# Performance work log

Measured on AMD Instinct MI355X. Metric: run time of the kernel, lower is better.

Reference implementation:

```python
import jax, jax.numpy as jnp
import numpy as np


def _rotate_half(x):
    a, b = jnp.split(x, 2, axis=-1)
    return jnp.concatenate([-b, a], axis=-1)


def _rope_tables(L, d, dtype):
    inv = 1.0 / (10000.0 ** (jnp.arange(0, d, 2, dtype=jnp.float32) / d))
    ang = jnp.arange(L, dtype=jnp.float32)[:, None] * inv[None, :]  # (L, d/2)
    cos = jnp.repeat(jnp.cos(ang), 2, axis=-1)[None, :, None, :].astype(dtype)  # (1,L,1,d)
    sin = jnp.repeat(jnp.sin(ang), 2, axis=-1)[None, :, None, :].astype(dtype)
    return cos, sin


def setup_inputs() -> dict:
    key = jax.random.key(0)
    ks = jax.random.split(key, 7)
    B, L, D, h = 1, 1024, 768, 12
    d = D // h
    s = 0.02
    return {
        "X": jax.random.normal(ks[0], (B, L, D), jnp.float32),
        "Wq": jax.random.normal(ks[1], (D, D), jnp.float32) * s,
        "Wk": jax.random.normal(ks[2], (D, D), jnp.float32) * s,
        "Wv": jax.random.normal(ks[3], (D, D), jnp.float32) * s,
        "Wu": jax.random.normal(ks[4], (D, D), jnp.float32) * s,
        "Wg": jax.random.normal(ks[5], (3 * h, D), jnp.float32) * s,
        "Wo": jax.random.normal(ks[6], (D, D), jnp.float32) * s,
        "prior_mu": jnp.zeros((1, 1, h, d), jnp.float32),
        "prior_log_tau": jnp.zeros((1, 1, h, 1), jnp.float32),
    }


def _forward(X, Wq, Wk, Wv, Wu, Wg, Wo, prior_mu, prior_log_tau):
    B, L, D = X.shape
    h = prior_mu.shape[2]
    d = D // h
    eps = 1e-12
    # projections (torch Linear: x @ W.T, no bias)
    q = (X @ Wq.T).reshape(B, L, h, d)
    k = (X @ Wk.T).reshape(B, L, h, d)
    v = (X @ Wv.T).reshape(B, L, h, d)
    u = (X @ Wu.T).reshape(B, L, h, d)
    gate = (X @ Wg.T).reshape(B, L, h, 3)
    t = jnp.arange(1, L + 1, dtype=X.dtype).reshape(1, L, 1, 1)
    # calculate_logit (logit_type='deviation', causal)
    log_tau = jnp.exp(jnp.clip(prior_log_tau, -50.0, 30.0))
    u_sum = jnp.cumsum(u, axis=1)
    bar_u = (log_tau * prior_mu + u_sum) / (log_tau + t)
    s_i = -jnp.sum(u * bar_u, axis=-1, keepdims=True) / np.float32(np.sqrt(d))  # (B,L,h,1)
    # RoPE + L2 normalize q, k
    cos, sin = _rope_tables(L, d, X.dtype)
    q = q * cos + _rotate_half(q) * sin
    k = k * cos + _rotate_half(k) * sin
    q = q / jnp.maximum(jnp.linalg.norm(q, axis=-1, keepdims=True), eps)
    k = k / jnp.maximum(jnp.linalg.norm(k, axis=-1, keepdims=True), eps)
    # associative causal branch of compute_o
    s_max = jax.lax.stop_gradient(jnp.max(s_i, axis=1, keepdims=True))
    exp_s = jnp.exp(s_i - s_max)              # (B,L,h,1)
    E_t = jnp.cumsum(exp_s, axis=1)
    P_t = jnp.cumsum(s_i, axis=1)
    kv = jnp.einsum('blhd,blhe->blhde', k, v)  # (B,L,h,d,d)
    F_t = jnp.cumsum(exp_s[..., None] * kv, axis=1)
    G_t = jnp.cumsum(s_i[..., None] * kv, axis=1)
    H_t = jnp.cumsum(kv, axis=1)
    sig1 = jax.nn.sigmoid(gate[..., 0:1])      # (B,L,h,1)
    sigh = jax.nn.sigmoid(gate[..., 1:2])
    alpha = sigh / (E_t + eps)
    beta = (sig1 - sigh) / t
    gamma = -((beta * P_t + sigh) / t)
    M = alpha[..., None] * F_t + beta[..., None] * G_t + gamma[..., None] * H_t
    out = jnp.einsum('blhd,blhde->blhe', q, M)  # (B,L,h,d)
    # LayerNorm over head dim, eps=1e-5, no affine
    mu = jnp.mean(out, axis=-1, keepdims=True)
    var = jnp.mean(jnp.square(out - mu), axis=-1, keepdims=True)
    out = (out - mu) / jnp.sqrt(var + 1e-5)
    # output projection (dropout=0.0 -> identity)
    return out.reshape(B, L, D) @ Wo.T


def reference(X, Wq, Wk, Wv, Wu, Wg, Wo, prior_mu, prior_log_tau):
    return _forward(X, Wq, Wk, Wv, Wu, Wg, Wo, prior_mu, prior_log_tau)
```

## Files before the change

### kernel.cpp

```cpp
#include <hip/hip_runtime.h>
#include <hip/hip_bf16.h>
#include <math.h>

typedef __attribute__((ext_vector_type(8))) short bf16x8;
typedef __attribute__((ext_vector_type(4))) float f32x4;

#define SEQ 1024
#define DIM 768
#define NH 12
#define HD 64


__device__ __forceinline__ float wave_reduce_sum(float v) {
    for (int off = 1; off < 64; off <<= 1) v += __shfl_xor(v, off);
    return v;
}
__device__ __forceinline__ short f2bs(float x) {
    __hip_bfloat16 h = __float2bfloat16(x);
    return *reinterpret_cast<short*>(&h);
}
__device__ __forceinline__ float bs2f(short x) {
    __hip_bfloat16 h = *reinterpret_cast<__hip_bfloat16*>(&x);
    return (float)h;
}
__device__ __forceinline__ bf16x8 cvt8r(const float4& a, const float4& b) {
    bf16x8 r;
    r[0]=f2bs(a.x); r[1]=f2bs(a.y); r[2]=f2bs(a.z); r[3]=f2bs(a.w);
    r[4]=f2bs(b.x); r[5]=f2bs(b.y); r[6]=f2bs(b.z); r[7]=f2bs(b.w);
    return r;
}
__device__ __forceinline__ void async_copy16(const void* gptr, void* ldsbase, int lane) {
#if __has_builtin(__builtin_amdgcn_global_load_lds)
    __builtin_amdgcn_global_load_lds(
        (const __attribute__((address_space(1))) unsigned int*)gptr,
        (__attribute__((address_space(3))) unsigned int*)ldsbase, 16, 0, 0);
#else
    *(bf16x8*)((short*)ldsbase + lane*8) = *(const bf16x8*)gptr;
#endif
}

__global__ __launch_bounds__(256) void k_prep(const float* __restrict__ X,
    const float* __restrict__ Wq, const float* __restrict__ Wk,
    const float* __restrict__ Wv, const float* __restrict__ Wu,
    const float* __restrict__ Wg, const float* __restrict__ Wo,
    short* __restrict__ Xb, short* __restrict__ Wqb, short* __restrict__ Wkb,
    short* __restrict__ Wvb, short* __restrict__ Wub, short* __restrict__ Wgb,
    short* __restrict__ Wob, float2* __restrict__ rope)
{
    int seg = blockIdx.y;
    if (seg == 7) {
        int i = blockIdx.x*256 + threadIdx.x;
        if (i >= 32768) return;
        int l = i >> 5, i2 = i & 31;
        float inv = expf((float)i2 * (-9.210340371976184f / 32.f));
        float ang = (float)l * inv;
        float2 cs;
        cs.x = cosf(ang);
        cs.y = sinf(ang);
        rope[i] = cs;
        return;
    }
    const float* src; short* dst; int n8;
    switch (seg) {
        case 0: src = X;  dst = Xb;  n8 = 98304; break;
        case 1: src = Wq; dst = Wqb; n8 = 73728; break;
        case 2: src = Wk; dst = Wkb; n8 = 73728; break;
        case 3: src = Wv; dst = Wvb; n8 = 73728; break;
        case 4: src = Wu; dst = Wub; n8 = 73728; break;
        case 5: src = Wg; dst = Wgb; n8 = 3456;  break;
        default: src = Wo; dst = Wob; n8 = 73728; break;
    }
    int i = blockIdx.x*256 + threadIdx.x;
    if (i >= n8) return;
    const float* s = src + (size_t)i*8;
    *(bf16x8*)(dst + (size_t)i*8) = cvt8r(*(const float4*)s, *(const float4*)(s + 4));
}

__global__ __launch_bounds__(256, 3) void k_proj5(const short* __restrict__ Xb,
    const short* __restrict__ Wqb, const short* __restrict__ Wkb,
    const short* __restrict__ Wvb, const short* __restrict__ Wub,
    const short* __restrict__ Wgb,
    __hip_bfloat16* __restrict__ Qb, __hip_bfloat16* __restrict__ Kb,
    __hip_bfloat16* __restrict__ Vt, __hip_bfloat16* __restrict__ Ub,
    float* __restrict__ G, const float2* __restrict__ rope)
{
    int t = blockIdx.x;
    int mat, rt, ct;
    if (t < 288)      { int m3 = t/96; mat = (m3==2)?3:m3; int r = t%96; rt = r/6; ct = r%6; }
    else if (t < 384) { mat = 2; int r = t-288; rt = r/8; ct = r%8; }
    else              { mat = 4; rt = t-384; ct = 0; }

    __shared__ short lds[24576];

    int tid = threadIdx.x;
    int wv = tid>>6, lane = tid&63, g = lane>>4, n = lane&15;
    int wn = wv;

    const short* Asrc; const short* Bsrc; int arow0, brow0, Brows;
    if (mat == 2) { Asrc = Wvb; Bsrc = Xb; arow0 = rt*64; brow0 = ct*128; Brows = SEQ; }
    else {
        Asrc = Xb; arow0 = rt*64; brow0 = ct*128;
        Bsrc = (mat==0)?Wqb:(mat==1)?Wkb:(mat==3)?Wub:Wgb;
        Brows = (mat==4) ? 36 : DIM;
    }

    auto dma_step = [&](int buf, int k0) {
        short* Ab = lds + buf*4096;
        short* Bb = lds + 8192 + buf*8192;
        for (int p = 0; p < 2; ++p) {
            int sbase = p*256 + wv*64;
            int s = sbase + lane;
            int r = s >> 3, c = s & 7, cl = c ^ (r & 7);
            async_copy16(Asrc + (size_t)(arow0 + r)*DIM + k0 + cl*8, Ab + sbase*8, lane);
        }
        for (int p = 0; p < 4; ++p) {
            int sbase = p*256 + wv*64;
            int s = sbase + lane;
            int r = s >> 3, c = s & 7, cl = c ^ (r & 7);
            int gr = brow0 + r; if (gr >= Brows) gr = Brows - 1;
            async_copy16(Bsrc + (size_t)gr*DIM + k0 + cl*8, Bb + sbase*8, lane);
        }
    };

    f32x4 acc[4][2];
    for (int i=0;i<4;++i) for (int j=0;j<2;++j) acc[i][j] = (f32x4){0,0,0,0};

    dma_step(0, 0);
    for (int it = 0; it < 12; ++it) {
        __syncthreads();
        if (it < 11) dma_step(1 - (it & 1), (it + 1)*64);
        int buf = it & 1;
        const short* Ab = lds + buf*4096;
        const short* Bb = lds + 8192 + buf*8192;
        for (int ks = 0; ks < 2; ++ks) {
            int q = ks*4 + g;
            bf16x8 af[4], bfr[2];
            for (int i=0;i<4;++i)
                af[i] = *(const bf16x8*)(&Ab[((i*16+n)*8 + (q ^ (n&7)))*8]);
            for (int j=0;j<2;++j)
                bfr[j] = *(const bf16x8*)(&Bb[((wn*32+j*16+n)*8 + (q ^ (n&7)))*8]);
            for (int i=0;i<4;++i)
                for (int j=0;j<2;++j)
                    acc[i][j] = __builtin_amdgcn_mfma_f32_16x16x32_bf16(af[i], bfr[j], acc[i][j], 0,0,0);
        }
    }
    __syncthreads();

    if (mat == 4) {
        for (int i=0;i<4;++i) for (int j=0;j<2;++j) for (int r=0;r<4;++r) {
            int row = rt*64 + i*16 + g*4 + r;
            int col = wn*32 + j*16 + n;
            if (col < 36) G[(size_t)row*36 + col] = acc[i][j][r];
        }
        return;
    }

    short* C = lds;
    for (int i=0;i<4;++i) for (int j=0;j<2;++j) for (int r=0;r<4;++r)
        C[(i*16 + g*4 + r)*128 + wn*32 + j*16 + n] = f2bs(acc[i][j][r]);
    __syncthreads();

    if (mat == 2) {
        for (int k = 0; k < 16; ++k) {
            int row = k*4 + wv;
            unsigned int v = ((const unsigned int*)C)[row*64 + lane];
            ((unsigned int*)(Vt + (size_t)(rt*64 + row)*SEQ + ct*128))[lane] = v;
        }
    } else if (mat == 3) {
        for (int k = 0; k < 32; ++k) {
            int u = k*4 + wv;
            int row = u >> 1, hsel = u & 1;
            Ub[((size_t)(2*ct + hsel)*SEQ + rt*64 + row)*HD + lane] =
                *(__hip_bfloat16*)&C[row*128 + hsel*64 + lane];
        }
    } else {
        __hip_bfloat16* dst = (mat==0) ? Qb : Kb;
        int i2 = lane >> 1;
        for (int k = 0; k < 32; ++k) {
            int u = k*4 + wv;
            int row = u >> 1, hsel = u & 1;
            int l = rt*64 + row;
            float x = bs2f(C[row*128 + hsel*64 + lane]);
            float2 cs = rope[l*32 + i2];
            float p = __shfl(x, lane ^ 32);
            float rot = (lane < 32) ? -p : p;
            float y = x*cs.x + rot*cs.y;
            float nrm = wave_reduce_sum(y*y);
            y = y / fmaxf(sqrtf(nrm), 1e-12f);
            dst[((size_t)(2*ct + hsel)*SEQ + l)*HD + lane] = __float2bfloat16(y);
        }
    }
}

__global__ __launch_bounds__(256) void k_si(const __hip_bfloat16* __restrict__ Ub,
    const float* __restrict__ pmu, const float* __restrict__ plt,
    float* __restrict__ si_)
{
    int T = blockIdx.x, h = blockIdx.y;
    int wv = threadIdx.x >> 6, lane = threadIdx.x & 63;
    int g = lane >> 4, n = lane & 15;
    int lbase = T*64 + wv*16;
    const short* ub = (const short*)Ub + (size_t)h*SEQ*HD;

    bf16x8 a0 = *(const bf16x8*)(ub + (size_t)(lbase + n)*HD + g*8);
    bf16x8 a1 = *(const bf16x8*)(ub + (size_t)(lbase + n)*HD + 32 + g*8);

    float ltv = fminf(fmaxf(plt[h], -50.f), 30.f);
    float ltau = expf(ltv);

    float p[4];
    for (int r = 0; r < 4; ++r) {
        int l = lbase + g*4 + r;
        float acc = 0.f;
        for (int c = n; c < 64; c += 16)
            acc += bs2f(ub[(size_t)l*HD + c]) * pmu[h*HD + c];
        p[r] = ltau * acc;
    }

    int diag = 4*T + wv;
    for (int jt = 0; jt < diag; ++jt) {
        const short* br = ub + (size_t)(jt*16 + n)*HD + g*8;
        bf16x8 b0 = *(const bf16x8*)br;
        bf16x8 b1 = *(const bf16x8*)(br + 32);
        f32x4 sacc = {0.f,0.f,0.f,0.f};
        sacc = __builtin_amdgcn_mfma_f32_16x16x32_bf16(a0, b0, sacc, 0,0,0);
        sacc = __builtin_amdgcn_mfma_f32_16x16x32_bf16(a1, b1, sacc, 0,0,0);
        for (int r = 0; r < 4; ++r) p[r] += sacc[r];
    }
    {
        const short* br = ub + (size_t)(diag*16 + n)*HD + g*8;
        bf16x8 b0 = *(const bf16x8*)br;
        bf16x8 b1 = *(const bf16x8*)(br + 32);
        f32x4 sacc = {0.f,0.f,0.f,0.f};
        sacc = __builtin_amdgcn_mfma_f32_16x16x32_bf16(a0, b0, sacc, 0,0,0);
        sacc = __builtin_amdgcn_mfma_f32_16x16x32_bf16(a1, b1, sacc, 0,0,0);
        for (int r = 0; r < 4; ++r) if (n <= g*4 + r) p[r] += sacc[r];
    }
    for (int off = 1; off < 16; off <<= 1)
        for (int r = 0; r < 4; ++r) p[r] += __shfl_xor(p[r], off);

    if (n == 0) {
        for (int r = 0; r < 4; ++r) {
            int l = lbase + g*4 + r;
            si_[h*SEQ + l] = -p[r] * 0.125f / (ltau + (float)(l + 1));
        }
    }
}

__global__ __launch_bounds__(64) void k_scan2(const float* __restrict__ G,
    const float* __restrict__ si_, float* __restrict__ es_,
    float* __restrict__ al_, float* __restrict__ be_, float* __restrict__ ga_)
{
    int h = blockIdx.x, lane = threadIdx.x;
    const float* si = si_ + h*SEQ;
    int base = lane * 16;
    float sv[16], ev[16];
    float vm = -1e30f;
#pragma unroll
    for (int i = 0; i < 16; ++i) { sv[i] = si[base + i]; vm = fmaxf(vm, sv[i]); }
    for (int off = 1; off < 64; off <<= 1) vm = fmaxf(vm, __shfl_xor(vm, off));
    float se = 0.f, ss = 0.f;
#pragma unroll
    for (int i = 0; i < 16; ++i) {
        ev[i] = expf(fminf(sv[i] - vm, 0.f));
        se += ev[i]; ss += sv[i];
    }
    float pe = se, ps = ss;
    for (int off = 1; off < 64; off <<= 1) {
        float t1 = __shfl_up(pe, off), t2 = __shfl_up(ps, off);
        if (lane >= off) { pe += t1; ps += t2; }
    }
    float E = pe - se, P = ps - ss;
#pragma unroll
    for (int i = 0; i < 16; ++i) {
        int l = base + i;
        E += ev[i]; P += sv[i];
        float t = (float)(l + 1);
        float s1 = 1.f / (1.f + expf(-G[(size_t)l*36 + h*3 + 0]));
        float sh = 1.f / (1.f + expf(-G[(size_t)l*36 + h*3 + 1]));
        float a = sh / (E + 1e-12f);
        float b = (s1 - sh) / t;
        float gm = -((b * P + sh) / t);
        es_[h*SEQ + l] = ev[i];
        al_[h*SEQ + l] = a;
        be_[h*SEQ + l] = b;
        ga_[h*SEQ + l] = gm;
    }
}

__global__ __launch_bounds__(256) void k_attn(const __hip_bfloat16* __restrict__ Qb,
    const __hip_bfloat16* __restrict__ Kb, const __hip_bfloat16* __restrict__ Vt,
    const float* __restrict__ si_, const float* __restrict__ es_,
    const float* __restrict__ al_, const float* __restrict__ be_,
    const float* __restrict__ ga_, __hip_bfloat16* __restrict__ opre)
{
    int t = blockIdx.x, h = blockIdx.y;
    int wv = threadIdx.x >> 6, lane = threadIdx.x & 63;
    int g = lane >> 4, n = lane & 15;
    __shared__ short P[4][16*64];
    __shared__ float Op[4][16][64];
    short* Pw = P[wv];
    int m0 = t*16;
    const short* qrow = (const short*)Qb + ((size_t)h*SEQ + m0 + n)*HD + g*8;
    bf16x8 qa0 = *(const bf16x8*)qrow;
    bf16x8 qa1 = *(const bf16x8*)(qrow + 32);
    const float* al = al_ + h*SEQ;
    const float* be = be_ + h*SEQ;
    const float* ga = ga_ + h*SEQ;
    const float* es = es_ + h*SEQ;
    const float* si = si_ + h*SEQ;
    float A_[4], B_[4], G_[4];
    for (int r = 0; r < 4; ++r) {
        int m = m0 + g*4 + r;
        A_[r] = al[m]; B_[r] = be[m]; G_[r] = ga[m];
    }
    f32x4 acco[4];
    for (int et = 0; et < 4; ++et) acco[et] = (f32x4){0.f,0.f,0.f,0.f};

    int jtmax = t >> 2;
    for (int jt = wv; jt <= jtmax; jt += 4) {
        int j0 = jt*64;
        for (int ct = 0; ct < 4; ++ct) {
            const short* krow = (const short*)Kb + ((size_t)h*SEQ + j0 + ct*16 + n)*HD + g*8;
            bf16x8 kb0 = *(const bf16x8*)krow;
            bf16x8 kb1 = *(const bf16x8*)(krow + 32);
            f32x4 sacc = {0.f,0.f,0.f,0.f};
            sacc = __builtin_amdgcn_mfma_f32_16x16x32_bf16(qa0, kb0, sacc, 0, 0, 0);
            sacc = __builtin_amdgcn_mfma_f32_16x16x32_bf16(qa1, kb1, sacc, 0, 0, 0);
            int j = j0 + ct*16 + n;
            float ej = es[j], sj = si[j];
            int chunk = ct*2 + (n>>3), e = n&7;
            for (int r = 0; r < 4; ++r) {
                int m = m0 + g*4 + r;
                float w = (j <= m) ? (A_[r]*ej + B_[r]*sj + G_[r]) : 0.f;
                int ml = g*4 + r;
                Pw[ml*64 + (chunk ^ (ml&7))*8 + e] = f2bs(w * sacc[r]);
            }
        }
        const short* vb = (const short*)Vt + (size_t)h*HD*SEQ;
        for (int et = 0; et < 4; ++et) {
            for (int sub = 0; sub < 2; ++sub) {
                int q = sub*4 + g;
                bf16x8 pa = *(const bf16x8*)(&Pw[n*64 + (q ^ (n&7))*8]);
                bf16x8 vfr = *(const bf16x8*)(vb + (size_t)(et*16 + n)*SEQ + j0 + sub*32 + g*8);
                acco[et] = __builtin_amdgcn_mfma_f32_16x16x32_bf16(pa, vfr, acco[et], 0, 0, 0);
            }
        }
    }
    for (int et = 0; et < 4; ++et)
        for (int r = 0; r < 4; ++r)
            Op[wv][g*4 + r][et*16 + n] = acco[et][r];
    __syncthreads();
    for (int rr = 0; rr < 4; ++rr) {
        int row = wv*4 + rr;
        float v = Op[0][row][lane] + Op[1][row][lane] + Op[2][row][lane] + Op[3][row][lane];
        float sm = wave_reduce_sum(v);
        float sq = wave_reduce_sum(v*v);
        float mu = sm * (1.f/64.f);
        float var = fmaxf(sq * (1.f/64.f) - mu*mu, 0.f);
        float invs = rsqrtf(var + 1e-5f);
        opre[(size_t)(m0 + row)*DIM + h*HD + lane] = __float2bfloat16((v - mu) * invs);
    }
}

__global__ __launch_bounds__(256, 4) void k_oproj(const short* __restrict__ A,
    const short* __restrict__ Wob, float* __restrict__ out)
{
    int rt = blockIdx.x, ct = blockIdx.y;
    __shared__ short lds[16384];

    int tid = threadIdx.x;
    int wv = tid>>6, lane = tid&63, g = lane>>4, n = lane&15;
    int wm = wv>>1, wn = wv&1;

    auto dma_step = [&](int buf, int k0) {
        short* Ab = lds + buf*4096;
        short* Bb = lds + 8192 + buf*4096;
        for (int p = 0; p < 2; ++p) {
            int sbase = p*256 + wv*64;
            int s = sbase + lane;
            int r = s >> 3, c = s & 7, cl = c ^ (r & 7);
            async_copy16(A + (size_t)(rt*64 + r)*DIM + k0 + cl*8, Ab + sbase*8, lane);
            async_copy16(Wob + (size_t)(ct*64 + r)*DIM + k0 + cl*8, Bb + sbase*8, lane);
        }
    };

    f32x4 acc[2][2];
    for (int i=0;i<2;++i) for (int j=0;j<2;++j) acc[i][j] = (f32x4){0,0,0,0};

    dma_step(0, 0);
    for (int it = 0; it < 12; ++it) {
        __syncthreads();
        if (it < 11) dma_step(1 - (it & 1), (it + 1)*64);
        int buf = it & 1;
        const short* Ab = lds + buf*4096;
        const short* Bb = lds + 8192 + buf*4096;
        for (int ks = 0; ks < 2; ++ks) {
            int q = ks*4 + g;
            bf16x8 af[2], bfr[2];
            for (int i=0;i<2;++i)
                af[i] = *(const bf16x8*)(&Ab[((wm*32+i*16+n)*8 + (q ^ (n&7)))*8]);
            for (int j=0;j<2;++j)
                bfr[j] = *(const bf16x8*)(&Bb[((wn*32+j*16+n)*8 + (q ^ (n&7)))*8]);
            for (int i=0;i<2;++i)
                for (int j=0;j<2;++j)
                    acc[i][j] = __builtin_amdgcn_mfma_f32_16x16x32_bf16(af[i], bfr[j], acc[i][j], 0,0,0);
        }
    }
    for (int i=0;i<2;++i) for (int j=0;j<2;++j) for (int r=0;r<4;++r) {
        int row = rt*64 + wm*32 + i*16 + g*4 + r;
        int col = ct*64 + wn*32 + j*16 + n;
        out[(size_t)row*DIM + col] = acc[i][j][r];
    }
}

extern "C" void kernel_launch(void* const* d_in, const int* in_sizes, int n_in,
                              void* d_out, int out_size, void* d_ws, size_t ws_size,
                              hipStream_t stream) {
    const float* X   = (const float*)d_in[0];
    const float* Wq  = (const float*)d_in[1];
    const float* Wk  = (const float*)d_in[2];
    const float* Wv  = (const float*)d_in[3];
    const float* Wu  = (const float*)d_in[4];
    const float* Wg  = (const float*)d_in[5];
    const float* Wo  = (const float*)d_in[6];
    const float* pmu = (const float*)d_in[7];
    const float* plt = (const float*)d_in[8];

    char* w = (char*)d_ws;
    __hip_bfloat16* Qb   = (__hip_bfloat16*)(w + 0);
    __hip_bfloat16* Kb   = (__hip_bfloat16*)(w + 1572864);
    __hip_bfloat16* Vt   = (__hip_bfloat16*)(w + 3145728);
    __hip_bfloat16* opre = (__hip_bfloat16*)(w + 4718592);
    float*          G    = (float*)(w + 6291456);
    float*          si_  = (float*)(w + 6438912);
    float*          es_  = si_ + NH*SEQ;
    float*          al_  = es_ + NH*SEQ;
    float*          be_  = al_ + NH*SEQ;
    float*          ga_  = be_ + NH*SEQ;
    short*          Xb   = (short*)(w + 6684672);
    short*          Wqb  = (short*)(w + 8257536);
    short*          Wkb  = (short*)(w + 9437184);
    short*          Wvb  = (short*)(w + 10616832);
    short*          Wub  = (short*)(w + 11796480);
    short*          Wgb  = (short*)(w + 12976128);
    short*          Wob  = (short*)(w + 13031424);
    float2*         rope = (float2*)(w + 14680064);
    __hip_bfloat16* Ub   = (__hip_bfloat16*)d_out;
    float*          out  = (float*)d_out;

    hipLaunchKernelGGL(k_prep, dim3(384, 8), dim3(256), 0, stream,
                       X, Wq, Wk, Wv, Wu, Wg, Wo, Xb, Wqb, Wkb, Wvb, Wub, Wgb, Wob, rope);
    hipLaunchKernelGGL(k_proj5, dim3(400), dim3(256), 0, stream,
                       Xb, Wqb, Wkb, Wvb, Wub, Wgb, Qb, Kb, Vt, Ub, G, rope);
    hipLaunchKernelGGL(k_si, dim3(16, NH), dim3(256), 0, stream,
                       Ub, pmu, plt, si_);
    hipLaunchKernelGGL(k_scan2, dim3(NH), dim3(64), 0, stream,
                       G, si_, es_, al_, be_, ga_);
    hipLaunchKernelGGL(k_attn, dim3(64, NH), dim3(256), 0, stream,
                       Qb, Kb, Vt, si_, es_, al_, be_, ga_, opre);
    hipLaunchKernelGGL(k_oproj, dim3(16, 12), dim3(256), 0, stream,
                       (const short*)opre, Wob, out);
}
```

Baseline: 161.6 us.

## Fuse fp32-to-bf16 conversion into GEMM loads and merge s_i with scan kernel

Removes the separate prep kernel that converted X and all weights to bf16 and built a RoPE table. The projection and output GEMMs now load fp32 directly into registers and convert while writing to LDS, and RoPE angles are generated in-kernel with a sincos recurrence. The s_i computation and the prefix scan are merged into one 1024-thread block per head, cutting two launches and their intermediate traffic. The trade-offs are synchronous register staging in place of async LDS DMA, twice the global bytes per GEMM tile, accumulated drift in the sincos recurrence, and only 12 blocks for the fused scan.

```diff
diff --git a/kernel.cpp b/kernel.cpp
--- a/kernel.cpp
+++ b/kernel.cpp
@@ -39,50 +39,13 @@
 #endif
 }
 
-__global__ __launch_bounds__(256) void k_prep(const float* __restrict__ X,
+__global__ __launch_bounds__(256, 3) void k_proj5(const float* __restrict__ Xf,
     const float* __restrict__ Wq, const float* __restrict__ Wk,
     const float* __restrict__ Wv, const float* __restrict__ Wu,
-    const float* __restrict__ Wg, const float* __restrict__ Wo,
-    short* __restrict__ Xb, short* __restrict__ Wqb, short* __restrict__ Wkb,
-    short* __restrict__ Wvb, short* __restrict__ Wub, short* __restrict__ Wgb,
-    short* __restrict__ Wob, float2* __restrict__ rope)
-{
-    int seg = blockIdx.y;
-    if (seg == 7) {
-        int i = blockIdx.x*256 + threadIdx.x;
-        if (i >= 32768) return;
-        int l = i >> 5, i2 = i & 31;
-        float inv = expf((float)i2 * (-9.210340371976184f / 32.f));
-        float ang = (float)l * inv;
-        float2 cs;
-        cs.x = cosf(ang);
-        cs.y = sinf(ang);
-        rope[i] = cs;
-        return;
-    }
-    const float* src; short* dst; int n8;
-    switch (seg) {
-        case 0: src = X;  dst = Xb;  n8 = 98304; break;
-        case 1: src = Wq; dst = Wqb; n8 = 73728; break;
-        case 2: src = Wk; dst = Wkb; n8 = 73728; break;
-        case 3: src = Wv; dst = Wvb; n8 = 73728; break;
-        case 4: src = Wu; dst = Wub; n8 = 73728; break;
-        case 5: src = Wg; dst = Wgb; n8 = 3456;  break;
-        default: src = Wo; dst = Wob; n8 = 73728; break;
-    }
-    int i = blockIdx.x*256 + threadIdx.x;
-    if (i >= n8) return;
-    const float* s = src + (size_t)i*8;
-    *(bf16x8*)(dst + (size_t)i*8) = cvt8r(*(const float4*)s, *(const float4*)(s + 4));
-}
-
-__global__ __launch_bounds__(256, 3) void k_proj5(const short* __restrict__ Xb,
-    const short* __restrict__ Wqb, const short* __restrict__ Wkb,
-    const short* __restrict__ Wvb, const short* __restrict__ Wub,
-    const short* __restrict__ Wgb,
+    const float* __restrict__ Wg,
     __hip_bfloat16* __restrict__ Qb, __hip_bfloat16* __restrict__ Kb,
     __hip_bfloat16* __restrict__ Vt, __hip_bfloat16* __restrict__ Ub,
-    float* __restrict__ G, const float2* __restrict__ rope)
+    float* __restrict__ G)
 {
     int t = blockIdx.x;
     int mat, rt, ct;
@@ -96,39 +59,56 @@
     int wv = tid>>6, lane = tid&63, g = lane>>4, n = lane&15;
     int wn = wv;
 
-    const short* Asrc; const short* Bsrc; int arow0, brow0, Brows;
-    if (mat == 2) { Asrc = Wvb; Bsrc = Xb; arow0 = rt*64; brow0 = ct*128; Brows = SEQ; }
+    const float* Asrc; const float* Bsrc; int arow0, brow0, Brows;
+    if (mat == 2) { Asrc = Wv; Bsrc = Xf; arow0 = rt*64; brow0 = ct*128; Brows = SEQ; }
     else {
-        Asrc = Xb; arow0 = rt*64; brow0 = ct*128;
-        Bsrc = (mat==0)?Wqb:(mat==1)?Wkb:(mat==3)?Wub:Wgb;
+        Asrc = Xf; arow0 = rt*64; brow0 = ct*128;
+        Bsrc = (mat==0)?Wq:(mat==1)?Wk:(mat==3)?Wu:Wg;
         Brows = (mat==4) ? 36 : DIM;
     }
 
-    auto dma_step = [&](int buf, int k0) {
-        short* Ab = lds + buf*4096;
-        short* Bb = lds + 8192 + buf*8192;
+    float4 ra[2][2], rb[4][2];
+    auto load_step = [&](int k0) {
+#pragma unroll
         for (int p = 0; p < 2; ++p) {
-            int sbase = p*256 + wv*64;
-            int s = sbase + lane;
+            int s = p*256 + wv*64 + lane;
             int r = s >> 3, c = s & 7, cl = c ^ (r & 7);
-            async_copy16(Asrc + (size_t)(arow0 + r)*DIM + k0 + cl*8, Ab + sbase*8, lane);
-        }
+            const float* sp = Asrc + (size_t)(arow0 + r)*DIM + k0 + cl*8;
+            ra[p][0] = *(const float4*)sp; ra[p][1] = *(const float4*)(sp + 4);
+        }
+#pragma unroll
         for (int p = 0; p < 4; ++p) {
-            int sbase = p*256 + wv*64;
-            int s = sbase + lane;
+            int s = p*256 + wv*64 + lane;
             int r = s >> 3, c = s & 7, cl = c ^ (r & 7);
             int gr = brow0 + r; if (gr >= Brows) gr = Brows - 1;
-            async_copy16(Bsrc + (size_t)gr*DIM + k0 + cl*8, Bb + sbase*8, lane);
+            const float* sp = Bsrc + (size_t)gr*DIM + k0 + cl*8;
+            rb[p][0] = *(const float4*)sp; rb[p][1] = *(const float4*)(sp + 4);
+        }
+    };
+    auto writeA = [&](int buf) {
+        short* Ab = lds + buf*4096;
+#pragma unroll
+        for (int p = 0; p < 2; ++p) {
+            int s = p*256 + wv*64 + lane;
+            *(bf16x8*)(Ab + s*8) = cvt8r(ra[p][0], ra[p][1]);
+        }
+    };
+    auto writeB = [&](int buf) {
+        short* Bb = lds + 8192 + buf*8192;
+#pragma unroll
+        for (int p = 0; p < 4; ++p) {
+            int s = p*256 + wv*64 + lane;
+            *(bf16x8*)(Bb + s*8) = cvt8r(rb[p][0], rb[p][1]);
         }
     };
 
     f32x4 acc[4][2];
     for (int i=0;i<4;++i) for (int j=0;j<2;++j) acc[i][j] = (f32x4){0,0,0,0};
 
-    dma_step(0, 0);
+    load_step(0); writeA(0); writeB(0);
     for (int it = 0; it < 12; ++it) {
         __syncthreads();
-        if (it < 11) dma_step(1 - (it & 1), (it + 1)*64);
+        if (it < 11) { load_step((it + 1)*64); writeA(1 - (it & 1)); }
         int buf = it & 1;
         const short* Ab = lds + buf*4096;
         const short* Bb = lds + 8192 + buf*8192;
@@ -143,6 +123,7 @@
                 for (int j=0;j<2;++j)
                     acc[i][j] = __builtin_amdgcn_mfma_f32_16x16x32_bf16(af[i], bfr[j], acc[i][j], 0,0,0);
         }
+        if (it < 11) writeB(1 - (it & 1));
     }
     __syncthreads();
 
@@ -176,88 +157,89 @@
     } else {
         __hip_bfloat16* dst = (mat==0) ? Qb : Kb;
         int i2 = lane >> 1;
+        int b = wv >> 1, hsel = wv & 1;
+        float inv = expf((float)i2 * (-9.210340371976184f / 32.f));
+        float c0, s0, C2, S2;
+        sincosf((float)(rt*64 + b) * inv, &s0, &c0);
+        sincosf(2.f * inv, &S2, &C2);
         for (int k = 0; k < 32; ++k) {
-            int u = k*4 + wv;
-            int row = u >> 1, hsel = u & 1;
+            int row = 2*k + b;
             int l = rt*64 + row;
             float x = bs2f(C[row*128 + hsel*64 + lane]);
-            float2 cs = rope[l*32 + i2];
             float p = __shfl(x, lane ^ 32);
             float rot = (lane < 32) ? -p : p;
-            float y = x*cs.x + rot*cs.y;
+            float y = x*c0 + rot*s0;
             float nrm = wave_reduce_sum(y*y);
             y = y / fmaxf(sqrtf(nrm), 1e-12f);
             dst[((size_t)(2*ct + hsel)*SEQ + l)*HD + lane] = __float2bfloat16(y);
-        }
-    }
-}
-
-__global__ __launch_bounds__(256) void k_si(const __hip_bfloat16* __restrict__ Ub,
-    const float* __restrict__ pmu, const float* __restrict__ plt,
-    float* __restrict__ si_)
+            float cn = c0*C2 - s0*S2;
+            s0 = s0*C2 + c0*S2;
+            c0 = cn;
+        }
+    }
+}
+
+__global__ __launch_bounds__(1024) void k_sscan(const __hip_bfloat16* __restrict__ Ub,
+    const float* __restrict__ Gm, const float* __restrict__ pmu,
+    const float* __restrict__ plt,
+    float* __restrict__ si_, float* __restrict__ es_, float* __restrict__ al_,
+    float* __restrict__ be_, float* __restrict__ ga_)
 {
-    int T = blockIdx.x, h = blockIdx.y;
-    int wv = threadIdx.x >> 6, lane = threadIdx.x & 63;
-    int g = lane >> 4, n = lane & 15;
-    int lbase = T*64 + wv*16;
+    int h = blockIdx.x;
+    int tid = threadIdx.x, wv = tid >> 6, lane = tid & 63, g = lane >> 4, n = lane & 15;
+    __shared__ float sbuf[SEQ];
     const short* ub = (const short*)Ub + (size_t)h*SEQ*HD;
-
-    bf16x8 a0 = *(const bf16x8*)(ub + (size_t)(lbase + n)*HD + g*8);
-    bf16x8 a1 = *(const bf16x8*)(ub + (size_t)(lbase + n)*HD + 32 + g*8);
-
     float ltv = fminf(fmaxf(plt[h], -50.f), 30.f);
     float ltau = expf(ltv);
 
-    float p[4];
-    for (int r = 0; r < 4; ++r) {
-        int l = lbase + g*4 + r;
-        float acc = 0.f;
-        for (int c = n; c < 64; c += 16)
-            acc += bs2f(ub[(size_t)l*HD + c]) * pmu[h*HD + c];
-        p[r] = ltau * acc;
-    }
-
-    int diag = 4*T + wv;
-    for (int jt = 0; jt < diag; ++jt) {
-        const short* br = ub + (size_t)(jt*16 + n)*HD + g*8;
-        bf16x8 b0 = *(const bf16x8*)br;
-        bf16x8 b1 = *(const bf16x8*)(br + 32);
-        f32x4 sacc = {0.f,0.f,0.f,0.f};
-        sacc = __builtin_amdgcn_mfma_f32_16x16x32_bf16(a0, b0, sacc, 0,0,0);
-        sacc = __builtin_amdgcn_mfma_f32_16x16x32_bf16(a1, b1, sacc, 0,0,0);
-        for (int r = 0; r < 4; ++r) p[r] += sacc[r];
-    }
-    {
-        const short* br = ub + (size_t)(diag*16 + n)*HD + g*8;
-        bf16x8 b0 = *(const bf16x8*)br;
-        bf16x8 b1 = *(const bf16x8*)(br + 32);
-        f32x4 sacc = {0.f,0.f,0.f,0.f};
-        sacc = __builtin_amdgcn_mfma_f32_16x16x32_bf16(a0, b0, sacc, 0,0,0);
-        sacc = __builtin_amdgcn_mfma_f32_16x16x32_bf16(a1, b1, sacc, 0,0,0);
-        for (int r = 0; r < 4; ++r) if (n <= g*4 + r) p[r] += sacc[r];
-    }
-    for (int off = 1; off < 16; off <<= 1)
-        for (int r = 0; r < 4; ++r) p[r] += __shfl_xor(p[r], off);
-
-    if (n == 0) {
+    for (int tt = 0; tt < 4; ++tt) {
+        int rt16 = tt*16 + wv;
+        int lbase = rt16*16;
+        bf16x8 a0 = *(const bf16x8*)(ub + (size_t)(lbase + n)*HD + g*8);
+        bf16x8 a1 = *(const bf16x8*)(ub + (size_t)(lbase + n)*HD + 32 + g*8);
+        f32x4 accA = (f32x4){0,0,0,0}, accB = (f32x4){0,0,0,0};
+        for (int jt = 0; jt < rt16; ++jt) {
+            const short* br = ub + (size_t)(jt*16 + n)*HD + g*8;
+            bf16x8 b0 = *(const bf16x8*)br;
+            bf16x8 b1 = *(const bf16x8*)(br + 32);
+            accA = __builtin_amdgcn_mfma_f32_16x16x32_bf16(a0, b0, accA, 0,0,0);
+            accB = __builtin_amdgcn_mfma_f32_16x16x32_bf16(a1, b1, accB, 0,0,0);
+        }
+        float p[4];
         for (int r = 0; r < 4; ++r) {
             int l = lbase + g*4 + r;
-            si_[h*SEQ + l] = -p[r] * 0.125f / (ltau + (float)(l + 1));
-        }
-    }
-}
-
-__global__ __launch_bounds__(64) void k_scan2(const float* __restrict__ G,
-    const float* __restrict__ si_, float* __restrict__ es_,
-    float* __restrict__ al_, float* __restrict__ be_, float* __restrict__ ga_)
-{
-    int h = blockIdx.x, lane = threadIdx.x;
-    const float* si = si_ + h*SEQ;
+            float acc = 0.f;
+            for (int c = n; c < 64; c += 16)
+                acc += bs2f(ub[(size_t)l*HD + c]) * pmu[h*HD + c];
+            p[r] = ltau*acc + accA[r] + accB[r];
+        }
+        {
+            const short* br = ub + (size_t)(lbase + n)*HD + g*8;
+            bf16x8 b0 = *(const bf16x8*)br;
+            bf16x8 b1 = *(const bf16x8*)(br + 32);
+            f32x4 d = (f32x4){0,0,0,0};
+            d = __builtin_amdgcn_mfma_f32_16x16x32_bf16(a0, b0, d, 0,0,0);
+            d = __builtin_amdgcn_mfma_f32_16x16x32_bf16(a1, b1, d, 0,0,0);
+            for (int r = 0; r < 4; ++r) if (n <= g*4 + r) p[r] += d[r];
+        }
+        for (int off = 1; off < 16; off <<= 1)
+            for (int r = 0; r < 4; ++r) p[r] += __shfl_xor(p[r], off);
+        if (n == 0) {
+            for (int r = 0; r < 4; ++r) {
+                int l = lbase + g*4 + r;
+                float v = -p[r] * 0.125f / (ltau + (float)(l + 1));
+                sbuf[l] = v;
+                si_[h*SEQ + l] = v;
+            }
+        }
+    }
+    __syncthreads();
+    if (wv != 0) return;
     int base = lane * 16;
     float sv[16], ev[16];
     float vm = -1e30f;
 #pragma unroll
-    for (int i = 0; i < 16; ++i) { sv[i] = si[base + i]; vm = fmaxf(vm, sv[i]); }
+    for (int i = 0; i < 16; ++i) { sv[i] = sbuf[base + i]; vm = fmaxf(vm, sv[i]); }
     for (int off = 1; off < 64; off <<= 1) vm = fmaxf(vm, __shfl_xor(vm, off));
     float se = 0.f, ss = 0.f;
 #pragma unroll
@@ -276,8 +258,8 @@
         int l = base + i;
         E += ev[i]; P += sv[i];
         float t = (float)(l + 1);
-        float s1 = 1.f / (1.f + expf(-G[(size_t)l*36 + h*3 + 0]));
-        float sh = 1.f / (1.f + expf(-G[(size_t)l*36 + h*3 + 1]));
+        float s1 = 1.f / (1.f + expf(-Gm[(size_t)l*36 + h*3 + 0]));
+        float sh = 1.f / (1.f + expf(-Gm[(size_t)l*36 + h*3 + 1]));
         float a = sh / (E + 1e-12f);
         float b = (s1 - sh) / t;
         float gm = -((b * P + sh) / t);
@@ -364,7 +346,7 @@
 }
 
 __global__ __launch_bounds__(256, 4) void k_oproj(const short* __restrict__ A,
-    const short* __restrict__ Wob, float* __restrict__ out)
+    const float* __restrict__ Wo, float* __restrict__ out)
 {
     int rt = blockIdx.x, ct = blockIdx.y;
     __shared__ short lds[16384];
@@ -373,25 +355,42 @@
     int wv = tid>>6, lane = tid&63, g = lane>>4, n = lane&15;
     int wm = wv>>1, wn = wv&1;
 
-    auto dma_step = [&](int buf, int k0) {
+    float4 rb[2][2];
+    auto dmaA = [&](int buf, int k0) {
         short* Ab = lds + buf*4096;
-        short* Bb = lds + 8192 + buf*4096;
+#pragma unroll
         for (int p = 0; p < 2; ++p) {
             int sbase = p*256 + wv*64;
             int s = sbase + lane;
             int r = s >> 3, c = s & 7, cl = c ^ (r & 7);
             async_copy16(A + (size_t)(rt*64 + r)*DIM + k0 + cl*8, Ab + sbase*8, lane);
-            async_copy16(Wob + (size_t)(ct*64 + r)*DIM + k0 + cl*8, Bb + sbase*8, lane);
+        }
+    };
+    auto loadB = [&](int k0) {
+#pragma unroll
+        for (int p = 0; p < 2; ++p) {
+            int s = p*256 + wv*64 + lane;
+            int r = s >> 3, c = s & 7, cl = c ^ (r & 7);
+            const float* sp = Wo + (size_t)(ct*64 + r)*DIM + k0 + cl*8;
+            rb[p][0] = *(const float4*)sp; rb[p][1] = *(const float4*)(sp + 4);
+        }
+    };
+    auto writeB = [&](int buf) {
+        short* Bb = lds + 8192 + buf*4096;
+#pragma unroll
+        for (int p = 0; p < 2; ++p) {
+            int s = p*256 + wv*64 + lane;
+            *(bf16x8*)(Bb + s*8) = cvt8r(rb[p][0], rb[p][1]);
         }
     };
 
     f32x4 acc[2][2];
     for (int i=0;i<2;++i) for (int j=0;j<2;++j) acc[i][j] = (f32x4){0,0,0,0};
 
-    dma_step(0, 0);
+    dmaA(0, 0); loadB(0); writeB(0);
     for (int it = 0; it < 12; ++it) {
         __syncthreads();
-        if (it < 11) dma_step(1 - (it & 1), (it + 1)*64);
+        if (it < 11) { dmaA(1 - (it & 1), (it + 1)*64); loadB((it + 1)*64); }
         int buf = it & 1;
         const short* Ab = lds + buf*4096;
         const short* Bb = lds + 8192 + buf*4096;
@@ -406,6 +405,7 @@
                 for (int j=0;j<2;++j)
                     acc[i][j] = __builtin_amdgcn_mfma_f32_16x16x32_bf16(af[i], bfr[j], acc[i][j], 0,0,0);
         }
+        if (it < 11) writeB(1 - (it & 1));
     }
     for (int i=0;i<2;++i) for (int j=0;j<2;++j) for (int r=0;r<4;++r) {
         int row = rt*64 + wm*32 + i*16 + g*4 + r;
@@ -438,27 +438,15 @@
     float*          al_  = es_ + NH*SEQ;
     float*          be_  = al_ + NH*SEQ;
     float*          ga_  = be_ + NH*SEQ;
-    short*          Xb   = (short*)(w + 6684672);
-    short*          Wqb  = (short*)(w + 8257536);
-    short*          Wkb  = (short*)(w + 9437184);
-    short*          Wvb  = (short*)(w + 10616832);
-    short*          Wub  = (short*)(w + 11796480);
-    short*          Wgb  = (short*)(w + 12976128);
-    short*          Wob  = (short*)(w + 13031424);
-    float2*         rope = (float2*)(w + 14680064);
     __hip_bfloat16* Ub   = (__hip_bfloat16*)d_out;
     float*          out  = (float*)d_out;
 
-    hipLaunchKernelGGL(k_prep, dim3(384, 8), dim3(256), 0, stream,
-                       X, Wq, Wk, Wv, Wu, Wg, Wo, Xb, Wqb, Wkb, Wvb, Wub, Wgb, Wob, rope);
     hipLaunchKernelGGL(k_proj5, dim3(400), dim3(256), 0, stream,
-                       Xb, Wqb, Wkb, Wvb, Wub, Wgb, Qb, Kb, Vt, Ub, G, rope);
-    hipLaunchKernelGGL(k_si, dim3(16, NH), dim3(256), 0, stream,
-                       Ub, pmu, plt, si_);
-    hipLaunchKernelGGL(k_scan2, dim3(NH), dim3(64), 0, stream,
-                       G, si_, es_, al_, be_, ga_);
+                       X, Wq, Wk, Wv, Wu, Wg, Qb, Kb, Vt, Ub, G);
+    hipLaunchKernelGGL(k_sscan, dim3(NH), dim3(1024), 0, stream,
+                       Ub, G, pmu, plt, si_, es_, al_, be_, ga_);
     hipLaunchKernelGGL(k_attn, dim3(64, NH), dim3(256), 0, stream,
                        Qb, Kb, Vt, si_, es_, al_, be_, ga_, opre);
     hipLaunchKernelGGL(k_oproj, dim3(16, 12), dim3(256), 0, stream,
-                       (const short*)opre, Wob, out);
-}
+                       (const short*)opre, Wo, out);
+}
```

Measured after the change: 260.0 us. 60.9% more time.

## Fuse s_i computation with scan kernel and compute RoPE angles on the fly

Applied to the files above, without the earlier changes.

Merges the s_i kernel (previously 16x12 blocks) and the per-head scan kernel into one kernel with one block per head. Each block computes s_i into shared memory and then runs the scan from it, which removes one launch and a global round trip for s_i. It also drops the precomputed RoPE table from the prep kernel. Each Q/K row instead gets its cos/sin from sincosf plus an angle-addition recurrence, removing the table writes and reads. The cost is far less parallelism for s_i: only 12 blocks, each looping serially over all row tiles. The recurrence also adds a small numerical drift.

```diff
diff --git a/kernel.cpp b/kernel.cpp
--- a/kernel.cpp
+++ b/kernel.cpp
@@ -45,21 +45,9 @@
     const float* __restrict__ Wg, const float* __restrict__ Wo,
     short* __restrict__ Xb, short* __restrict__ Wqb, short* __restrict__ Wkb,
     short* __restrict__ Wvb, short* __restrict__ Wub, short* __restrict__ Wgb,
-    short* __restrict__ Wob, float2* __restrict__ rope)
+    short* __restrict__ Wob)
 {
     int seg = blockIdx.y;
-    if (seg == 7) {
-        int i = blockIdx.x*256 + threadIdx.x;
-        if (i >= 32768) return;
-        int l = i >> 5, i2 = i & 31;
-        float inv = expf((float)i2 * (-9.210340371976184f / 32.f));
-        float ang = (float)l * inv;
-        float2 cs;
-        cs.x = cosf(ang);
-        cs.y = sinf(ang);
-        rope[i] = cs;
-        return;
-    }
     const float* src; short* dst; int n8;
     switch (seg) {
         case 0: src = X;  dst = Xb;  n8 = 98304; break;
@@ -82,7 +70,7 @@
     const short* __restrict__ Wgb,
     __hip_bfloat16* __restrict__ Qb, __hip_bfloat16* __restrict__ Kb,
     __hip_bfloat16* __restrict__ Vt, __hip_bfloat16* __restrict__ Ub,
-    float* __restrict__ G, const float2* __restrict__ rope)
+    float* __restrict__ G)
 {
     int t = blockIdx.x;
     int mat, rt, ct;
@@ -176,88 +164,89 @@
     } else {
         __hip_bfloat16* dst = (mat==0) ? Qb : Kb;
         int i2 = lane >> 1;
+        int b = wv >> 1, hsel = wv & 1;
+        float inv = expf((float)i2 * (-9.210340371976184f / 32.f));
+        float c0, s0, C2, S2;
+        sincosf((float)(rt*64 + b) * inv, &s0, &c0);
+        sincosf(2.f * inv, &S2, &C2);
         for (int k = 0; k < 32; ++k) {
-            int u = k*4 + wv;
-            int row = u >> 1, hsel = u & 1;
+            int row = 2*k + b;
             int l = rt*64 + row;
             float x = bs2f(C[row*128 + hsel*64 + lane]);
-            float2 cs = rope[l*32 + i2];
             float p = __shfl(x, lane ^ 32);
             float rot = (lane < 32) ? -p : p;
-            float y = x*cs.x + rot*cs.y;
+            float y = x*c0 + rot*s0;
             float nrm = wave_reduce_sum(y*y);
             y = y / fmaxf(sqrtf(nrm), 1e-12f);
             dst[((size_t)(2*ct + hsel)*SEQ + l)*HD + lane] = __float2bfloat16(y);
-        }
-    }
-}
-
-__global__ __launch_bounds__(256) void k_si(const __hip_bfloat16* __restrict__ Ub,
-    const float* __restrict__ pmu, const float* __restrict__ plt,
-    float* __restrict__ si_)
+            float cn = c0*C2 - s0*S2;
+            s0 = s0*C2 + c0*S2;
+            c0 = cn;
+        }
+    }
+}
+
+__global__ __launch_bounds__(256, 1) void k_siscan(const __hip_bfloat16* __restrict__ Ub,
+    const float* __restrict__ Gm, const float* __restrict__ pmu,
+    const float* __restrict__ plt,
+    float* __restrict__ si_, float* __restrict__ es_, float* __restrict__ al_,
+    float* __restrict__ be_, float* __restrict__ ga_)
 {
-    int T = blockIdx.x, h = blockIdx.y;
-    int wv = threadIdx.x >> 6, lane = threadIdx.x & 63;
-    int g = lane >> 4, n = lane & 15;
-    int lbase = T*64 + wv*16;
+    int h = blockIdx.x;
+    int tid = threadIdx.x, wv = tid >> 6, lane = tid & 63, g = lane >> 4, n = lane & 15;
+    __shared__ float sbuf[SEQ];
     const short* ub = (const short*)Ub + (size_t)h*SEQ*HD;
-
-    bf16x8 a0 = *(const bf16x8*)(ub + (size_t)(lbase + n)*HD + g*8);
-    bf16x8 a1 = *(const bf16x8*)(ub + (size_t)(lbase + n)*HD + 32 + g*8);
-
     float ltv = fminf(fmaxf(plt[h], -50.f), 30.f);
     float ltau = expf(ltv);
 
-    float p[4];
-    for (int r = 0; r < 4; ++r) {
-        int l = lbase + g*4 + r;
-        float acc = 0.f;
-        for (int c = n; c < 64; c += 16)
-            acc += bs2f(ub[(size_t)l*HD + c]) * pmu[h*HD + c];
-        p[r] = ltau * acc;
-    }
-
-    int diag = 4*T + wv;
-    for (int jt = 0; jt < diag; ++jt) {
-        const short* br = ub + (size_t)(jt*16 + n)*HD + g*8;
-        bf16x8 b0 = *(const bf16x8*)br;
-        bf16x8 b1 = *(const bf16x8*)(br + 32);
-        f32x4 sacc = {0.f,0.f,0.f,0.f};
-        sacc = __builtin_amdgcn_mfma_f32_16x16x32_bf16(a0, b0, sacc, 0,0,0);
-        sacc = __builtin_amdgcn_mfma_f32_16x16x32_bf16(a1, b1, sacc, 0,0,0);
-        for (int r = 0; r < 4; ++r) p[r] += sacc[r];
-    }
-    {
-        const short* br = ub + (size_t)(diag*16 + n)*HD + g*8;
-        bf16x8 b0 = *(const bf16x8*)br;
-        bf16x8 b1 = *(const bf16x8*)(br + 32);
-        f32x4 sacc = {0.f,0.f,0.f,0.f};
-        sacc = __builtin_amdgcn_mfma_f32_16x16x32_bf16(a0, b0, sacc, 0,0,0);
-        sacc = __builtin_amdgcn_mfma_f32_16x16x32_bf16(a1, b1, sacc, 0,0,0);
-        for (int r = 0; r < 4; ++r) if (n <= g*4 + r) p[r] += sacc[r];
-    }
-    for (int off = 1; off < 16; off <<= 1)
-        for (int r = 0; r < 4; ++r) p[r] += __shfl_xor(p[r], off);
-
-    if (n == 0) {
+    for (int tt = 0; tt < 16; ++tt) {
+        int rt16 = tt*4 + wv;
+        int lbase = rt16*16;
+        bf16x8 a0 = *(const bf16x8*)(ub + (size_t)(lbase + n)*HD + g*8);
+        bf16x8 a1 = *(const bf16x8*)(ub + (size_t)(lbase + n)*HD + 32 + g*8);
+        f32x4 accA = (f32x4){0,0,0,0}, accB = (f32x4){0,0,0,0};
+        for (int jt = 0; jt < rt16; ++jt) {
+            const short* br = ub + (size_t)(jt*16 + n)*HD + g*8;
+            bf16x8 b0 = *(const bf16x8*)br;
+            bf16x8 b1 = *(const bf16x8*)(br + 32);
+            accA = __builtin_amdgcn_mfma_f32_16x16x32_bf16(a0, b0, accA, 0,0,0);
+            accB = __builtin_amdgcn_mfma_f32_16x16x32_bf16(a1, b1, accB, 0,0,0);
+        }
+        float p[4];
         for (int r = 0; r < 4; ++r) {
             int l = lbase + g*4 + r;
-            si_[h*SEQ + l] = -p[r] * 0.125f / (ltau + (float)(l + 1));
-        }
-    }
-}
-
-__global__ __launch_bounds__(64) void k_scan2(const float* __restrict__ G,
-    const float* __restrict__ si_, float* __restrict__ es_,
-    float* __restrict__ al_, float* __restrict__ be_, float* __restrict__ ga_)
-{
-    int h = blockIdx.x, lane = threadIdx.x;
-    const float* si = si_ + h*SEQ;
+            float acc = 0.f;
+            for (int c = n; c < 64; c += 16)
+                acc += bs2f(ub[(size_t)l*HD + c]) * pmu[h*HD + c];
+            p[r] = ltau*acc + accA[r] + accB[r];
+        }
+        {
+            const short* br = ub + (size_t)(lbase + n)*HD + g*8;
+            bf16x8 b0 = *(const bf16x8*)br;
+            bf16x8 b1 = *(const bf16x8*)(br + 32);
+            f32x4 d = (f32x4){0,0,0,0};
+            d = __builtin_amdgcn_mfma_f32_16x16x32_bf16(a0, b0, d, 0,0,0);
+            d = __builtin_amdgcn_mfma_f32_16x16x32_bf16(a1, b1, d, 0,0,0);
+            for (int r = 0; r < 4; ++r) if (n <= g*4 + r) p[r] += d[r];
+        }
+        for (int off = 1; off < 16; off <<= 1)
+            for (int r = 0; r < 4; ++r) p[r] += __shfl_xor(p[r], off);
+        if (n == 0) {
+            for (int r = 0; r < 4; ++r) {
+                int l = lbase + g*4 + r;
+                float v = -p[r] * 0.125f / (ltau + (float)(l + 1));
+                sbuf[l] = v;
+                si_[h*SEQ + l] = v;
+            }
+        }
+    }
+    __syncthreads();
+    if (wv != 0) return;
     int base = lane * 16;
     float sv[16], ev[16];
     float vm = -1e30f;
 #pragma unroll
-    for (int i = 0; i < 16; ++i) { sv[i] = si[base + i]; vm = fmaxf(vm, sv[i]); }
+    for (int i = 0; i < 16; ++i) { sv[i] = sbuf[base + i]; vm = fmaxf(vm, sv[i]); }
     for (int off = 1; off < 64; off <<= 1) vm = fmaxf(vm, __shfl_xor(vm, off));
     float se = 0.f, ss = 0.f;
 #pragma unroll
@@ -276,8 +265,8 @@
         int l = base + i;
         E += ev[i]; P += sv[i];
         float t = (float)(l + 1);
-        float s1 = 1.f / (1.f + expf(-G[(size_t)l*36 + h*3 + 0]));
-        float sh = 1.f / (1.f + expf(-G[(size_t)l*36 + h*3 + 1]));
+        float s1 = 1.f / (1.f + expf(-Gm[(size_t)l*36 + h*3 + 0]));
+        float sh = 1.f / (1.f + expf(-Gm[(size_t)l*36 + h*3 + 1]));
         float a = sh / (E + 1e-12f);
         float b = (s1 - sh) / t;
         float gm = -((b * P + sh) / t);
@@ -445,18 +434,15 @@
     short*          Wub  = (short*)(w + 11796480);
     short*          Wgb  = (short*)(w + 12976128);
     short*          Wob  = (short*)(w + 13031424);
-    float2*         rope = (float2*)(w + 14680064);
     __hip_bfloat16* Ub   = (__hip_bfloat16*)d_out;
     float*          out  = (float*)d_out;
 
-    hipLaunchKernelGGL(k_prep, dim3(384, 8), dim3(256), 0, stream,
-                       X, Wq, Wk, Wv, Wu, Wg, Wo, Xb, Wqb, Wkb, Wvb, Wub, Wgb, Wob, rope);
+    hipLaunchKernelGGL(k_prep, dim3(384, 7), dim3(256), 0, stream,
+                       X, Wq, Wk, Wv, Wu, Wg, Wo, Xb, Wqb, Wkb, Wvb, Wub, Wgb, Wob);
     hipLaunchKernelGGL(k_proj5, dim3(400), dim3(256), 0, stream,
-                       Xb, Wqb, Wkb, Wvb, Wub, Wgb, Qb, Kb, Vt, Ub, G, rope);
-    hipLaunchKernelGGL(k_si, dim3(16, NH), dim3(256), 0, stream,
-                       Ub, pmu, plt, si_);
-    hipLaunchKernelGGL(k_scan2, dim3(NH), dim3(64), 0, stream,
-                       G, si_, es_, al_, be_, ga_);
+                       Xb, Wqb, Wkb, Wvb, Wub, Wgb, Qb, Kb, Vt, Ub, G);
+    hipLaunchKernelGGL(k_siscan, dim3(NH), dim3(256), 0, stream,
+                       Ub, G, pmu, plt, si_, es_, al_, be_, ga_);
     hipLaunchKernelGGL(k_attn, dim3(64, NH), dim3(256), 0, stream,
                        Qb, Kb, Vt, si_, es_, al_, be_, ga_, opre);
     hipLaunchKernelGGL(k_oproj, dim3(16, 12), dim3(256), 0, stream,
```

Measured after the change: 279.5 us. 1.73x slower.
